# Kernel optimization log

Measured on AMD Instinct MI355X. Metric: run time of the kernel, lower is better.

The kernel has to match this reference:

```python
import jax, jax.numpy as jnp
import numpy as np

C = 32
KSHAPE = (C, C, 3, 3)  # (C_out, C_in, kH, kW)
BN_EPS = 1e-5


def _binary_act(x):
    # forward: sign(x); backward: identity clipped to |x|<1 (STE)
    xc = jnp.clip(x, -1.0, 1.0)
    return jax.lax.stop_gradient(jnp.sign(x) - xc) + xc


def _binarize_weight(w_flat, shape):
    w = w_flat.reshape(shape)
    scale = jax.lax.stop_gradient(jnp.mean(jnp.abs(w)))  # global scalar scale, detached
    wc = jnp.clip(w, -1.0, 1.0)
    # forward: scale*sign(w); backward flows through clamp(w,-1,1)
    return jax.lax.stop_gradient(scale * jnp.sign(w) - wc) + wc


def _bi_conv_bn(x, w_flat, gamma, beta, stride):
    xb = _binary_act(x)
    w = _binarize_weight(w_flat, KSHAPE)
    y = jax.lax.conv_general_dilated(
        xb, w, window_strides=(stride, stride), padding=[(1, 1), (1, 1)],
        dimension_numbers=('NCHW', 'OIHW', 'NCHW'))
    # BatchNorm2d in training mode (batch stats, biased variance)
    m = jnp.mean(y, axis=(0, 2, 3), keepdims=True)
    v = jnp.mean((y - m) ** 2, axis=(0, 2, 3), keepdims=True)
    yhat = (y - m) * jax.lax.rsqrt(v + BN_EPS)
    return gamma.reshape(1, -1, 1, 1) * yhat + beta.reshape(1, -1, 1, 1)


def setup_inputs() -> dict:
    key = jax.random.key(0)
    k1, k2, k3 = jax.random.split(key, 3)
    return {
        'x': jax.random.normal(k1, (32, C, 160, 160), dtype=jnp.float32),
        'w1': jax.random.normal(k2, (C * C * 9, 1), dtype=jnp.float32) * 0.05,
        'gamma1': jnp.ones((C,), dtype=jnp.float32),
        'beta1': jnp.zeros((C,), dtype=jnp.float32),
        'w2': jax.random.normal(k3, (C * C * 9, 1), dtype=jnp.float32) * 0.05,
        'gamma2': jnp.ones((C,), dtype=jnp.float32),
        'beta2': jnp.zeros((C,), dtype=jnp.float32),
    }


def reference(x, w1, gamma1, beta1, w2, gamma2, beta2):
    # bireal residual block, stride=1 => skip_op is Identity
    inner = _bi_conv_bn(x, w1, gamma1, beta1, 1) + x
    out = _bi_conv_bn(inner, w2, gamma2, beta2, 1) + inner
    return out
```

## Files before the change

### kernel.cpp

```cpp
#include <hip/hip_runtime.h>
#include <stdint.h>

#define NIMG 32
#define CH 32
#define HH 160
#define WW 160
#define HWL (HH*WW)
#define PRS 164
#define PHH 162
#define PIMG (PHH*PRS)
#define NPIX (NIMG*HWL)
#define HALO_WORDS 968

#define OFF_P     0
#define OFF_P2    3400704
#define OFF_INNER (OFF_P2 + 3400704)
#define OFF_WP    (OFF_INNER + 52428800)
#define OFF_CORR  (OFF_WP + 2304)
#define OFF_SC    (OFF_CORR + 2304)
#define OFF_SB    (OFF_SC + 128)

struct StatLine {
  int s1; int pad0; unsigned long long s2; char pad[112];
};

__device__ __forceinline__ unsigned short f2bf(float f) {
  unsigned u = __float_as_uint(f);
  u += 0x7fffu + ((u >> 16) & 1u);
  return (unsigned short)(u >> 16);
}
__device__ __forceinline__ float bf2f(unsigned short u) {
  return __uint_as_float((uint32_t)u << 16);
}

__device__ __forceinline__ void conv4(const uint32_t r[3][6], const uint32_t* wsh,
                                      int co, int& a0, int& a1, int& a2, int& a3)
{
  a0 = a1 = a2 = a3 = 0;
  #pragma unroll
  for (int dy = 0; dy < 3; ++dy) {
    #pragma unroll
    for (int dx = 0; dx < 3; ++dx) {
      uint32_t wvv = wsh[co * 9 + dy * 3 + dx];
      a0 += __popc(r[dy][0 + dx] ^ wvv);
      a1 += __popc(r[dy][1 + dx] ^ wvv);
      a2 += __popc(r[dy][2 + dx] ^ wvv);
      a3 += __popc(r[dy][3 + dx] ^ wvv);
    }
  }
}

__global__ __launch_bounds__(256) void pack_prep(const float* __restrict__ x,
    const float* __restrict__ w1, const float* __restrict__ w2,
    uint32_t* __restrict__ P, uint32_t* __restrict__ P2, uint32_t* __restrict__ WP,
    int* __restrict__ CORR, float* __restrict__ SC, StatLine* __restrict__ SB)
{
  __shared__ float red[256];
  const int tid = threadIdx.x;
  const int b = blockIdx.x;

  if (b >= 800) {
    if (b == 800) {
      int* z = (int*)SB;
      for (int i = tid; i < 2048; i += 256) z[i] = 0;
      for (int cv = 0; cv < 2; ++cv) {
        const float* w = cv ? w2 : w1;
        float s = 0.f;
        for (int i = tid; i < 9216; i += 256) s += fabsf(w[i]);
        red[tid] = s;
        __syncthreads();
        for (int st = 128; st > 0; st >>= 1) {
          if (tid < st) red[tid] += red[tid + st];
          __syncthreads();
        }
        if (tid == 0) SC[cv] = red[0] / 9216.0f;
        for (int i = tid; i < 288; i += 256) {
          int co = i / 9, t = i - co * 9;
          uint32_t bw = 0;
          for (int ci = 0; ci < 32; ++ci)
            bw |= (w[(co * 32 + ci) * 9 + t] > 0.0f) ? (1u << ci) : 0u;
          WP[cv * 288 + i] = bw;
        }
        __syncthreads();
        for (int i = tid; i < 288; i += 256) {
          int cls = i / 32, co = i - cls * 32;
          int hc = cls / 3, wc = cls - hc * 3;
          int corr = 0;
          for (int t = 0; t < 9; ++t) {
            int dy = t / 3 - 1, dx = t % 3 - 1;
            bool inval = (hc == 0 && dy == -1) || (hc == 2 && dy == 1) ||
                         (wc == 0 && dx == -1) || (wc == 2 && dx == 1);
            if (inval) corr += 32 - 2 * __popc(WP[cv * 288 + co * 9 + t]);
          }
          CORR[cv * 288 + cls * 32 + co] = corr;
        }
        __syncthreads();
      }
    } else {
      int k = (b - 801) * 256 + tid;
      uint32_t* buf = (k < 32 * HALO_WORDS) ? P : P2;
      int j = k % (32 * HALO_WORDS);
      int img = j / HALO_WORDS;
      int r = j - img * HALO_WORDS;
      int pr, pc;
      if (r < 164)      { pr = 0;   pc = r; }
      else if (r < 328) { pr = 161; pc = r - 164; }
      else {
        int k2 = r - 328;
        pr = 1 + (k2 >> 2);
        int q = k2 & 3;
        pc = (q == 0) ? 0 : (160 + q);
      }
      buf[img * PIMG + pr * PRS + pc] = 0;
    }
    return;
  }

  int g = b * 256 + tid;
  int p0 = g * 4;
  int n = p0 / HWL;
  int i = p0 - n * HWL;
  const float* xb = x + (size_t)n * CH * HWL + i;
  uint32_t bb0 = 0, bb1 = 0, bb2 = 0, bb3 = 0;
  #pragma unroll
  for (int cg = 0; cg < 4; ++cg) {
    float4 v[8];
    #pragma unroll
    for (int j = 0; j < 8; ++j)
      v[j] = *reinterpret_cast<const float4*>(xb + (size_t)(cg * 8 + j) * HWL);
    #pragma unroll
    for (int j = 0; j < 8; ++j) {
      uint32_t m = 1u << (cg * 8 + j);
      if (v[j].x > 0.f) bb0 |= m;
      if (v[j].y > 0.f) bb1 |= m;
      if (v[j].z > 0.f) bb2 |= m;
      if (v[j].w > 0.f) bb3 |= m;
    }
  }
  int h = i / WW, w = i - (i / WW) * WW;
  uint32_t* pw = P + n * PIMG + (h + 1) * PRS + (w + 1);
  pw[0] = bb0; pw[1] = bb1; pw[2] = bb2; pw[3] = bb3;
}

__global__ __launch_bounds__(256) void conv_stats(const uint32_t* __restrict__ P,
    const uint32_t* __restrict__ WP, const int* __restrict__ CORR,
    StatLine* __restrict__ sb)
{
  __shared__ uint32_t wsh[288];
  __shared__ int csh[288];
  __shared__ int ls1[32], ls2[32];
  const int tid = threadIdx.x;
  for (int i = tid; i < 288; i += 256) { wsh[i] = WP[i]; csh[i] = CORR[i]; }
  if (tid < 32) { ls1[tid] = 0; ls2[tid] = 0; }
  __syncthreads();

  int g = blockIdx.x * 256 + tid;
  int w4 = g % 40;
  int t1 = g / 40;
  int h = t1 % 160;
  int n = t1 / 160;

  const uint32_t* base = P + n * PIMG + h * PRS + w4 * 4;
  uint32_t r[3][6];
  #pragma unroll
  for (int dy = 0; dy < 3; ++dy) {
    uint4 a = *reinterpret_cast<const uint4*>(base + dy * PRS);
    uint2 bw = *reinterpret_cast<const uint2*>(base + dy * PRS + 4);
    r[dy][0] = a.x; r[dy][1] = a.y; r[dy][2] = a.z; r[dy][3] = a.w;
    r[dy][4] = bw.x; r[dy][5] = bw.y;
  }

  int rowc = (h == 0) ? 0 : ((h == 159) ? 6 : 3);
  int cls0  = rowc + ((w4 == 0) ? 0 : 1);
  int cls12 = rowc + 1;
  int cls3  = rowc + ((w4 == 39) ? 2 : 1);
  int lane = tid & 63;

  #pragma unroll
  for (int co = 0; co < 32; ++co) {
    int a0, a1, a2, a3;
    conv4(r, wsh, co, a0, a1, a2, a3);
    int d0 = 288 - 2 * a0 - csh[cls0 * 32 + co];
    int d1 = 288 - 2 * a1 - csh[cls12 * 32 + co];
    int d2 = 288 - 2 * a2 - csh[cls12 * 32 + co];
    int d3 = 288 - 2 * a3 - csh[cls3 * 32 + co];
    int ds = d0 + d1 + d2 + d3;
    int sq = d0 * d0 + d1 * d1 + d2 * d2 + d3 * d3;
    #pragma unroll
    for (int off = 32; off > 0; off >>= 1) {
      ds += __shfl_down(ds, off);
      sq += __shfl_down(sq, off);
    }
    if (lane == 0) { atomicAdd(&ls1[co], ds); atomicAdd(&ls2[co], sq); }
  }
  __syncthreads();
  if (tid < 32) {
    atomicAdd(&sb[tid].s1, ls1[tid]);
    atomicAdd(&sb[tid].s2, (unsigned long long)(long long)ls2[tid]);
  }
}

__global__ __launch_bounds__(256) void conv_bn1(const uint32_t* __restrict__ P,
    const uint32_t* __restrict__ WP, const int* __restrict__ CORR,
    const float* __restrict__ x, const float* __restrict__ SCp,
    const StatLine* __restrict__ sb, const float* __restrict__ gamma,
    const float* __restrict__ beta, unsigned short* __restrict__ INNER,
    uint32_t* __restrict__ P2)
{
  __shared__ uint32_t wsh[288];
  __shared__ int csh[288];
  __shared__ float Ash[32], Bsh[32];
  const int tid = threadIdx.x;
  for (int i = tid; i < 288; i += 256) { wsh[i] = WP[i]; csh[i] = CORR[i]; }
  if (tid < 32) {
    double sc = (double)SCp[0];
    double m  = sc * (double)sb[tid].s1 / (double)NPIX;
    double ms = sc * sc * (double)(long long)sb[tid].s2 / (double)NPIX;
    float inv = (float)(1.0 / sqrt(ms - m * m + 1e-5));
    float gm = gamma[tid];
    Ash[tid] = gm * inv * (float)sc;
    Bsh[tid] = beta[tid] - gm * inv * (float)m;
  }
  __syncthreads();

  int g = blockIdx.x * 256 + tid;
  int w4 = g % 40;
  int t1 = g / 40;
  int h = t1 % 160;
  int n = t1 / 160;

  const uint32_t* base = P + n * PIMG + h * PRS + w4 * 4;
  uint32_t r[3][6];
  #pragma unroll
  for (int dy = 0; dy < 3; ++dy) {
    uint4 a = *reinterpret_cast<const uint4*>(base + dy * PRS);
    uint2 bw = *reinterpret_cast<const uint2*>(base + dy * PRS + 4);
    r[dy][0] = a.x; r[dy][1] = a.y; r[dy][2] = a.z; r[dy][3] = a.w;
    r[dy][4] = bw.x; r[dy][5] = bw.y;
  }
  int rowc = (h == 0) ? 0 : ((h == 159) ? 6 : 3);
  int cls0  = rowc + ((w4 == 0) ? 0 : 1);
  int cls12 = rowc + 1;
  int cls3  = rowc + ((w4 == 39) ? 2 : 1);

  int i = h * WW + w4 * 4;
  size_t pbase = (size_t)n * CH * HWL + i;
  uint32_t bb0 = 0, bb1 = 0, bb2 = 0, bb3 = 0;
  #pragma unroll
  for (int cg = 0; cg < 4; ++cg) {
    float4 xv[8];
    #pragma unroll
    for (int j = 0; j < 8; ++j)
      xv[j] = *reinterpret_cast<const float4*>(x + pbase + (size_t)(cg * 8 + j) * HWL);
    #pragma unroll
    for (int j = 0; j < 8; ++j) {
      int co = cg * 8 + j;
      int a0, a1, a2, a3;
      conv4(r, wsh, co, a0, a1, a2, a3);
      int d0 = 288 - 2 * a0 - csh[cls0 * 32 + co];
      int d1 = 288 - 2 * a1 - csh[cls12 * 32 + co];
      int d2 = 288 - 2 * a2 - csh[cls12 * 32 + co];
      int d3 = 288 - 2 * a3 - csh[cls3 * 32 + co];
      float A = Ash[co], Bv = Bsh[co];
      float v0 = fmaf(A, (float)d0, Bv) + xv[j].x;
      float v1 = fmaf(A, (float)d1, Bv) + xv[j].y;
      float v2 = fmaf(A, (float)d2, Bv) + xv[j].z;
      float v3 = fmaf(A, (float)d3, Bv) + xv[j].w;
      ushort4 o; o.x = f2bf(v0); o.y = f2bf(v1); o.z = f2bf(v2); o.w = f2bf(v3);
      *reinterpret_cast<ushort4*>(INNER + pbase + (size_t)co * HWL) = o;
      uint32_t m = 1u << co;
      if (v0 > 0.f) bb0 |= m;
      if (v1 > 0.f) bb1 |= m;
      if (v2 > 0.f) bb2 |= m;
      if (v3 > 0.f) bb3 |= m;
    }
  }
  uint32_t* pw = P2 + n * PIMG + (h + 1) * PRS + (w4 * 4 + 1);
  pw[0] = bb0; pw[1] = bb1; pw[2] = bb2; pw[3] = bb3;
}

__global__ __launch_bounds__(256) void conv_bn2(const uint32_t* __restrict__ P2,
    const uint32_t* __restrict__ WP, const int* __restrict__ CORR,
    const unsigned short* __restrict__ INNER, const float* __restrict__ SCp,
    const StatLine* __restrict__ sb, const float* __restrict__ gamma,
    const float* __restrict__ beta, float* __restrict__ out)
{
  __shared__ uint32_t wsh[288];
  __shared__ int csh[288];
  __shared__ float Ash[32], Bsh[32];
  const int tid = threadIdx.x;
  for (int i = tid; i < 288; i += 256) { wsh[i] = WP[i]; csh[i] = CORR[i]; }
  if (tid < 32) {
    double sc = (double)SCp[0];
    double m  = sc * (double)sb[tid].s1 / (double)NPIX;
    double ms = sc * sc * (double)(long long)sb[tid].s2 / (double)NPIX;
    float inv = (float)(1.0 / sqrt(ms - m * m + 1e-5));
    float gm = gamma[tid];
    Ash[tid] = gm * inv * (float)sc;
    Bsh[tid] = beta[tid] - gm * inv * (float)m;
  }
  __syncthreads();

  int g = blockIdx.x * 256 + tid;
  int w4 = g % 40;
  int t1 = g / 40;
  int h = t1 % 160;
  int n = t1 / 160;

  const uint32_t* base = P2 + n * PIMG + h * PRS + w4 * 4;
  uint32_t r[3][6];
  #pragma unroll
  for (int dy = 0; dy < 3; ++dy) {
    uint4 a = *reinterpret_cast<const uint4*>(base + dy * PRS);
    uint2 bw = *reinterpret_cast<const uint2*>(base + dy * PRS + 4);
    r[dy][0] = a.x; r[dy][1] = a.y; r[dy][2] = a.z; r[dy][3] = a.w;
    r[dy][4] = bw.x; r[dy][5] = bw.y;
  }
  int rowc = (h == 0) ? 0 : ((h == 159) ? 6 : 3);
  int cls0  = rowc + ((w4 == 0) ? 0 : 1);
  int cls12 = rowc + 1;
  int cls3  = rowc + ((w4 == 39) ? 2 : 1);

  int i = h * WW + w4 * 4;
  size_t pbase = (size_t)n * CH * HWL + i;
  #pragma unroll
  for (int cg = 0; cg < 4; ++cg) {
    ushort4 iv[8];
    #pragma unroll
    for (int j = 0; j < 8; ++j)
      iv[j] = *reinterpret_cast<const ushort4*>(INNER + pbase + (size_t)(cg * 8 + j) * HWL);
    #pragma unroll
    for (int j = 0; j < 8; ++j) {
      int co = cg * 8 + j;
      int a0, a1, a2, a3;
      conv4(r, wsh, co, a0, a1, a2, a3);
      int d0 = 288 - 2 * a0 - csh[cls0 * 32 + co];
      int d1 = 288 - 2 * a1 - csh[cls12 * 32 + co];
      int d2 = 288 - 2 * a2 - csh[cls12 * 32 + co];
      int d3 = 288 - 2 * a3 - csh[cls3 * 32 + co];
      float A = Ash[co], Bv = Bsh[co];
      float4 o;
      o.x = fmaf(A, (float)d0, Bv) + bf2f(iv[j].x);
      o.y = fmaf(A, (float)d1, Bv) + bf2f(iv[j].y);
      o.z = fmaf(A, (float)d2, Bv) + bf2f(iv[j].z);
      o.w = fmaf(A, (float)d3, Bv) + bf2f(iv[j].w);
      *reinterpret_cast<float4*>(out + pbase + (size_t)co * HWL) = o;
    }
  }
}

extern "C" void kernel_launch(void* const* d_in, const int* in_sizes, int n_in,
                              void* d_out, int out_size, void* d_ws, size_t ws_size,
                              hipStream_t stream)
{
  (void)in_sizes; (void)n_in; (void)out_size; (void)ws_size;
  const float* x  = (const float*)d_in[0];
  const float* w1 = (const float*)d_in[1];
  const float* g1 = (const float*)d_in[2];
  const float* b1 = (const float*)d_in[3];
  const float* w2 = (const float*)d_in[4];
  const float* g2 = (const float*)d_in[5];
  const float* b2 = (const float*)d_in[6];
  float* out = (float*)d_out;
  char* ws = (char*)d_ws;

  uint32_t*       P     = (uint32_t*)(ws + OFF_P);
  uint32_t*       P2    = (uint32_t*)(ws + OFF_P2);
  unsigned short* INNER = (unsigned short*)(ws + OFF_INNER);
  uint32_t*       WP    = (uint32_t*)(ws + OFF_WP);
  int*            CORR  = (int*)(ws + OFF_CORR);
  float*          SC    = (float*)(ws + OFF_SC);
  StatLine*       SB    = (StatLine*)(ws + OFF_SB);

  pack_prep<<<1043, 256, 0, stream>>>(x, w1, w2, P, P2, WP, CORR, SC, SB);
  conv_stats<<<800, 256, 0, stream>>>(P, WP, CORR, SB);
  conv_bn1<<<800, 256, 0, stream>>>(P, WP, CORR, x, SC, SB, g1, b1, INNER, P2);
  conv_stats<<<800, 256, 0, stream>>>(P2, WP + 288, CORR + 288, SB + 32);
  conv_bn2<<<800, 256, 0, stream>>>(P2, WP + 288, CORR + 288, INNER, SC + 1, SB + 32, g2, b2, out);
}
```

Measured before the change: 198.2 us.

## Split pack work across lanes and hoist all channel loads in BN kernels

The packing kernel now has four lanes share each 8-pixel group. Each lane loads 8 channels as two float4 reads per channel, and the sign bits are combined with xor-shuffles, doubling the grid and shortening each thread's load chain. Both fused conv+BN kernels now issue all 32 per-channel loads (x or the bf16 inner tensor) up front, before the popcount convolution loop, to raise memory-level parallelism. They also gain a `__launch_bounds__(256, 2)` occupancy hint. Holding 32 vectors in registers raises register pressure and may limit occupancy.

Result: slower. 205.0 us (+3.5%).

```diff
diff --git a/kernel.cpp b/kernel.cpp
--- a/kernel.cpp
+++ b/kernel.cpp
@@ -50,7 +50,7 @@
   }
 }
 
-__global__ __launch_bounds__(256) void pack_prep(const float* __restrict__ x,
+__global__ __launch_bounds__(256, 2) void pack_prep(const float* __restrict__ x,
     const float* __restrict__ w1, const float* __restrict__ w2,
     uint32_t* __restrict__ P, uint32_t* __restrict__ P2, uint32_t* __restrict__ WP,
     int* __restrict__ CORR, float* __restrict__ SC, StatLine* __restrict__ SB)
@@ -59,8 +59,8 @@
   const int tid = threadIdx.x;
   const int b = blockIdx.x;
 
-  if (b >= 800) {
-    if (b == 800) {
+  if (b >= 1600) {
+    if (b == 1842) {
       int* z = (int*)SB;
       for (int i = tid; i < 2048; i += 256) z[i] = 0;
       for (int cv = 0; cv < 2; ++cv) {
@@ -97,7 +97,7 @@
         __syncthreads();
       }
     } else {
-      int k = (b - 801) * 256 + tid;
+      int k = (b - 1600) * 256 + tid;
       uint32_t* buf = (k < 32 * HALO_WORDS) ? P : P2;
       int j = k % (32 * HALO_WORDS);
       int img = j / HALO_WORDS;
@@ -117,29 +117,56 @@
   }
 
   int g = b * 256 + tid;
-  int p0 = g * 4;
+  int grp = g >> 2;
+  int k = g & 3;
+  int p0 = grp * 8;
   int n = p0 / HWL;
   int i = p0 - n * HWL;
-  const float* xb = x + (size_t)n * CH * HWL + i;
-  uint32_t bb0 = 0, bb1 = 0, bb2 = 0, bb3 = 0;
-  #pragma unroll
-  for (int cg = 0; cg < 4; ++cg) {
-    float4 v[8];
-    #pragma unroll
-    for (int j = 0; j < 8; ++j)
-      v[j] = *reinterpret_cast<const float4*>(xb + (size_t)(cg * 8 + j) * HWL);
-    #pragma unroll
-    for (int j = 0; j < 8; ++j) {
-      uint32_t m = 1u << (cg * 8 + j);
-      if (v[j].x > 0.f) bb0 |= m;
-      if (v[j].y > 0.f) bb1 |= m;
-      if (v[j].z > 0.f) bb2 |= m;
-      if (v[j].w > 0.f) bb3 |= m;
-    }
-  }
+  const float* xb = x + (size_t)n * CH * HWL + i + (size_t)(k * 8) * HWL;
+  float4 a0 = *reinterpret_cast<const float4*>(xb + 0 * HWL);
+  float4 b0 = *reinterpret_cast<const float4*>(xb + 0 * HWL + 4);
+  float4 a1 = *reinterpret_cast<const float4*>(xb + 1 * HWL);
+  float4 b1 = *reinterpret_cast<const float4*>(xb + 1 * HWL + 4);
+  float4 a2 = *reinterpret_cast<const float4*>(xb + 2 * HWL);
+  float4 b2 = *reinterpret_cast<const float4*>(xb + 2 * HWL + 4);
+  float4 a3 = *reinterpret_cast<const float4*>(xb + 3 * HWL);
+  float4 b3 = *reinterpret_cast<const float4*>(xb + 3 * HWL + 4);
+  float4 a4 = *reinterpret_cast<const float4*>(xb + 4 * HWL);
+  float4 b4 = *reinterpret_cast<const float4*>(xb + 4 * HWL + 4);
+  float4 a5 = *reinterpret_cast<const float4*>(xb + 5 * HWL);
+  float4 b5 = *reinterpret_cast<const float4*>(xb + 5 * HWL + 4);
+  float4 a6 = *reinterpret_cast<const float4*>(xb + 6 * HWL);
+  float4 b6 = *reinterpret_cast<const float4*>(xb + 6 * HWL + 4);
+  float4 a7 = *reinterpret_cast<const float4*>(xb + 7 * HWL);
+  float4 b7 = *reinterpret_cast<const float4*>(xb + 7 * HWL + 4);
+
+  uint32_t q0 = 0, q1 = 0, q2 = 0, q3 = 0, q4 = 0, q5 = 0, q6 = 0, q7 = 0;
+  int c0 = k * 8;
+  #define ACC(j, aj, bj)                                        \
+    { uint32_t m = 1u << (c0 + j);                              \
+      if (aj.x > 0.f) q0 |= m; if (aj.y > 0.f) q1 |= m;         \
+      if (aj.z > 0.f) q2 |= m; if (aj.w > 0.f) q3 |= m;         \
+      if (bj.x > 0.f) q4 |= m; if (bj.y > 0.f) q5 |= m;         \
+      if (bj.z > 0.f) q6 |= m; if (bj.w > 0.f) q7 |= m; }
+  ACC(0, a0, b0) ACC(1, a1, b1) ACC(2, a2, b2) ACC(3, a3, b3)
+  ACC(4, a4, b4) ACC(5, a5, b5) ACC(6, a6, b6) ACC(7, a7, b7)
+  #undef ACC
+
+  q0 |= __shfl_xor(q0, 1); q1 |= __shfl_xor(q1, 1);
+  q2 |= __shfl_xor(q2, 1); q3 |= __shfl_xor(q3, 1);
+  q4 |= __shfl_xor(q4, 1); q5 |= __shfl_xor(q5, 1);
+  q6 |= __shfl_xor(q6, 1); q7 |= __shfl_xor(q7, 1);
+  q0 |= __shfl_xor(q0, 2); q1 |= __shfl_xor(q1, 2);
+  q2 |= __shfl_xor(q2, 2); q3 |= __shfl_xor(q3, 2);
+  q4 |= __shfl_xor(q4, 2); q5 |= __shfl_xor(q5, 2);
+  q6 |= __shfl_xor(q6, 2); q7 |= __shfl_xor(q7, 2);
+
   int h = i / WW, w = i - (i / WW) * WW;
   uint32_t* pw = P + n * PIMG + (h + 1) * PRS + (w + 1);
-  pw[0] = bb0; pw[1] = bb1; pw[2] = bb2; pw[3] = bb3;
+  uint32_t wa = (k == 0) ? q0 : (k == 1) ? q1 : (k == 2) ? q2 : q3;
+  uint32_t wb = (k == 0) ? q4 : (k == 1) ? q5 : (k == 2) ? q6 : q7;
+  pw[k] = wa;
+  pw[k + 4] = wb;
 }
 
 __global__ __launch_bounds__(256) void conv_stats(const uint32_t* __restrict__ P,
@@ -200,7 +227,7 @@
   }
 }
 
-__global__ __launch_bounds__(256) void conv_bn1(const uint32_t* __restrict__ P,
+__global__ __launch_bounds__(256, 2) void conv_bn1(const uint32_t* __restrict__ P,
     const uint32_t* __restrict__ WP, const int* __restrict__ CORR,
     const float* __restrict__ x, const float* __restrict__ SCp,
     const StatLine* __restrict__ sb, const float* __restrict__ gamma,
@@ -245,41 +272,39 @@
 
   int i = h * WW + w4 * 4;
   size_t pbase = (size_t)n * CH * HWL + i;
+
+  float4 xv[32];
+  #pragma unroll
+  for (int j = 0; j < 32; ++j)
+    xv[j] = *reinterpret_cast<const float4*>(x + pbase + (size_t)j * HWL);
+
   uint32_t bb0 = 0, bb1 = 0, bb2 = 0, bb3 = 0;
   #pragma unroll
-  for (int cg = 0; cg < 4; ++cg) {
-    float4 xv[8];
-    #pragma unroll
-    for (int j = 0; j < 8; ++j)
-      xv[j] = *reinterpret_cast<const float4*>(x + pbase + (size_t)(cg * 8 + j) * HWL);
-    #pragma unroll
-    for (int j = 0; j < 8; ++j) {
-      int co = cg * 8 + j;
-      int a0, a1, a2, a3;
-      conv4(r, wsh, co, a0, a1, a2, a3);
-      int d0 = 288 - 2 * a0 - csh[cls0 * 32 + co];
-      int d1 = 288 - 2 * a1 - csh[cls12 * 32 + co];
-      int d2 = 288 - 2 * a2 - csh[cls12 * 32 + co];
-      int d3 = 288 - 2 * a3 - csh[cls3 * 32 + co];
-      float A = Ash[co], Bv = Bsh[co];
-      float v0 = fmaf(A, (float)d0, Bv) + xv[j].x;
-      float v1 = fmaf(A, (float)d1, Bv) + xv[j].y;
-      float v2 = fmaf(A, (float)d2, Bv) + xv[j].z;
-      float v3 = fmaf(A, (float)d3, Bv) + xv[j].w;
-      ushort4 o; o.x = f2bf(v0); o.y = f2bf(v1); o.z = f2bf(v2); o.w = f2bf(v3);
-      *reinterpret_cast<ushort4*>(INNER + pbase + (size_t)co * HWL) = o;
-      uint32_t m = 1u << co;
-      if (v0 > 0.f) bb0 |= m;
-      if (v1 > 0.f) bb1 |= m;
-      if (v2 > 0.f) bb2 |= m;
-      if (v3 > 0.f) bb3 |= m;
-    }
+  for (int co = 0; co < 32; ++co) {
+    int a0, a1, a2, a3;
+    conv4(r, wsh, co, a0, a1, a2, a3);
+    int d0 = 288 - 2 * a0 - csh[cls0 * 32 + co];
+    int d1 = 288 - 2 * a1 - csh[cls12 * 32 + co];
+    int d2 = 288 - 2 * a2 - csh[cls12 * 32 + co];
+    int d3 = 288 - 2 * a3 - csh[cls3 * 32 + co];
+    float A = Ash[co], Bv = Bsh[co];
+    float v0 = fmaf(A, (float)d0, Bv) + xv[co].x;
+    float v1 = fmaf(A, (float)d1, Bv) + xv[co].y;
+    float v2 = fmaf(A, (float)d2, Bv) + xv[co].z;
+    float v3 = fmaf(A, (float)d3, Bv) + xv[co].w;
+    ushort4 o; o.x = f2bf(v0); o.y = f2bf(v1); o.z = f2bf(v2); o.w = f2bf(v3);
+    *reinterpret_cast<ushort4*>(INNER + pbase + (size_t)co * HWL) = o;
+    uint32_t m = 1u << co;
+    if (v0 > 0.f) bb0 |= m;
+    if (v1 > 0.f) bb1 |= m;
+    if (v2 > 0.f) bb2 |= m;
+    if (v3 > 0.f) bb3 |= m;
   }
   uint32_t* pw = P2 + n * PIMG + (h + 1) * PRS + (w4 * 4 + 1);
   pw[0] = bb0; pw[1] = bb1; pw[2] = bb2; pw[3] = bb3;
 }
 
-__global__ __launch_bounds__(256) void conv_bn2(const uint32_t* __restrict__ P2,
+__global__ __launch_bounds__(256, 2) void conv_bn2(const uint32_t* __restrict__ P2,
     const uint32_t* __restrict__ WP, const int* __restrict__ CORR,
     const unsigned short* __restrict__ INNER, const float* __restrict__ SCp,
     const StatLine* __restrict__ sb, const float* __restrict__ gamma,
@@ -323,29 +348,27 @@
 
   int i = h * WW + w4 * 4;
   size_t pbase = (size_t)n * CH * HWL + i;
-  #pragma unroll
-  for (int cg = 0; cg < 4; ++cg) {
-    ushort4 iv[8];
-    #pragma unroll
-    for (int j = 0; j < 8; ++j)
-      iv[j] = *reinterpret_cast<const ushort4*>(INNER + pbase + (size_t)(cg * 8 + j) * HWL);
-    #pragma unroll
-    for (int j = 0; j < 8; ++j) {
-      int co = cg * 8 + j;
-      int a0, a1, a2, a3;
-      conv4(r, wsh, co, a0, a1, a2, a3);
-      int d0 = 288 - 2 * a0 - csh[cls0 * 32 + co];
-      int d1 = 288 - 2 * a1 - csh[cls12 * 32 + co];
-      int d2 = 288 - 2 * a2 - csh[cls12 * 32 + co];
-      int d3 = 288 - 2 * a3 - csh[cls3 * 32 + co];
-      float A = Ash[co], Bv = Bsh[co];
-      float4 o;
-      o.x = fmaf(A, (float)d0, Bv) + bf2f(iv[j].x);
-      o.y = fmaf(A, (float)d1, Bv) + bf2f(iv[j].y);
-      o.z = fmaf(A, (float)d2, Bv) + bf2f(iv[j].z);
-      o.w = fmaf(A, (float)d3, Bv) + bf2f(iv[j].w);
-      *reinterpret_cast<float4*>(out + pbase + (size_t)co * HWL) = o;
-    }
+
+  ushort4 iv[32];
+  #pragma unroll
+  for (int j = 0; j < 32; ++j)
+    iv[j] = *reinterpret_cast<const ushort4*>(INNER + pbase + (size_t)j * HWL);
+
+  #pragma unroll
+  for (int co = 0; co < 32; ++co) {
+    int a0, a1, a2, a3;
+    conv4(r, wsh, co, a0, a1, a2, a3);
+    int d0 = 288 - 2 * a0 - csh[cls0 * 32 + co];
+    int d1 = 288 - 2 * a1 - csh[cls12 * 32 + co];
+    int d2 = 288 - 2 * a2 - csh[cls12 * 32 + co];
+    int d3 = 288 - 2 * a3 - csh[cls3 * 32 + co];
+    float A = Ash[co], Bv = Bsh[co];
+    float4 o;
+    o.x = fmaf(A, (float)d0, Bv) + bf2f(iv[co].x);
+    o.y = fmaf(A, (float)d1, Bv) + bf2f(iv[co].y);
+    o.z = fmaf(A, (float)d2, Bv) + bf2f(iv[co].z);
+    o.w = fmaf(A, (float)d3, Bv) + bf2f(iv[co].w);
+    *reinterpret_cast<float4*>(out + pbase + (size_t)co * HWL) = o;
   }
 }
 
@@ -372,7 +395,7 @@
   float*          SC    = (float*)(ws + OFF_SC);
   StatLine*       SB    = (StatLine*)(ws + OFF_SB);
 
-  pack_prep<<<1043, 256, 0, stream>>>(x, w1, w2, P, P2, WP, CORR, SC, SB);
+  pack_prep<<<1843, 256, 0, stream>>>(x, w1, w2, P, P2, WP, CORR, SC, SB);
   conv_stats<<<800, 256, 0, stream>>>(P, WP, CORR, SB);
   conv_bn1<<<800, 256, 0, stream>>>(P, WP, CORR, x, SC, SB, g1, b1, INNER, P2);
   conv_stats<<<800, 256, 0, stream>>>(P2, WP + 288, CORR + 288, SB + 32);
```
